# Kernel tuning notes

Measured on AMD Instinct MI355X. Metric: run time of the kernel, lower is better.

The kernel has to match this reference:

```python
import jax, jax.numpy as jnp
import numpy as np

N = 50000      # nodes
E = 800000     # directed edges (avg degree 16)
IN = 96
H = 96
OUT = 96


def _gcn(x, W, b, src, dst, norm, n):
    # PyG GCNConv: h = x @ W; aggregate norm * h[src] at dst; add bias.
    h = x @ W                          # [N, H]
    msg = h[src] * norm[:, None]       # [E+N, H]
    out = jax.ops.segment_sum(msg, dst, num_segments=n)
    return out + b


def setup_inputs() -> dict:
    key = jax.random.key(0)
    ks = jax.random.split(key, 12)
    s = 1.0 / np.sqrt(IN)
    sh = 1.0 / np.sqrt(H)
    return {
        "x": jax.random.normal(ks[0], (N, IN), dtype=jnp.float32),
        "edge_index": jax.random.randint(ks[1], (2, E), 0, N, dtype=jnp.int32),
        "W_local": jax.random.uniform(ks[2], (IN, H), jnp.float32, -s, s),
        "b_local": jnp.zeros((H,), jnp.float32),
        "W_g1": jax.random.uniform(ks[3], (IN, H), jnp.float32, -s, s),
        "b_g1": jnp.zeros((H,), jnp.float32),
        "W_g2": jax.random.uniform(ks[4], (H, H), jnp.float32, -sh, sh),
        "b_g2": jnp.zeros((H,), jnp.float32),
        "W_fuse": jax.random.uniform(ks[5], (2 * H, OUT), jnp.float32, -1.0 / np.sqrt(2 * H), 1.0 / np.sqrt(2 * H)),
        "b_fuse": jnp.zeros((OUT,), jnp.float32),
    }


def reference(x, edge_index, W_local, b_local, W_g1, b_g1, W_g2, b_g2, W_fuse, b_fuse):
    n = x.shape[0]
    loops = jnp.arange(n, dtype=edge_index.dtype)
    src = jnp.concatenate([edge_index[0], loops])   # add self-loops (GCNConv default)
    dst = jnp.concatenate([edge_index[1], loops])
    deg = jax.ops.segment_sum(jnp.ones_like(dst, dtype=x.dtype), dst, num_segments=n)
    dis = jax.lax.rsqrt(jnp.maximum(deg, 1.0))      # deg >= 1 due to self-loops
    norm = dis[src] * dis[dst]                      # sym-normalized edge weights

    local = jax.nn.relu(_gcn(x, W_local, b_local, src, dst, norm, n))
    g = jax.nn.relu(_gcn(x, W_g1, b_g1, src, dst, norm, n))
    g = jax.nn.relu(_gcn(g, W_g2, b_g2, src, dst, norm, n))

    combined = jnp.concatenate([local, g], axis=-1)  # [N, 2H]
    return combined @ W_fuse + b_fuse                # [N, OUT]
```

## Files before the change

### kernel.cpp

```cpp
#include <hip/hip_runtime.h>

#define HDIM 96
#define LSTR 104
#define CAP 96

typedef __attribute__((ext_vector_type(8))) short bf16x8;
typedef __attribute__((ext_vector_type(4))) float f32x4;

#define LGKM0() do { asm volatile("s_waitcnt lgkmcnt(0)" ::: "memory"); \
                     __builtin_amdgcn_sched_barrier(0); } while (0)

__device__ __forceinline__ unsigned short bf16rne(float x) {
  const unsigned u = __float_as_uint(x);
  return (unsigned short)((u + 0x7fff + ((u >> 16) & 1)) >> 16);
}

__device__ __forceinline__ void split2(float x, unsigned short& hi, unsigned short& lo) {
  const unsigned u = __float_as_uint(x);
  hi = (unsigned short)(u >> 16);
  const float xhi = __uint_as_float(u & 0xffff0000u);
  lo = (unsigned short)(__float_as_uint(x - xhi) >> 16);
}

__global__ __launch_bounds__(256) void init_k(
    int* __restrict__ indeg, int n, int zb,
    const float* __restrict__ W0, const float* __restrict__ W1,
    const float* __restrict__ W2, const float* __restrict__ W3,
    unsigned short* __restrict__ dH, unsigned short* __restrict__ dL) {
  if (blockIdx.x < zb) {
    const int i = blockIdx.x * 256 + threadIdx.x;
    if (i < n) indeg[i] = 0;
  } else {
    const int t = (blockIdx.x - zb) * 256 + threadIdx.x;
    if (t < 5 * 9216) {
      const int tile = t / 9216, r = t % 9216;
      const int nn = r / 96, k = r % 96;
      const float* W = (tile == 0) ? W0 : (tile == 1) ? W1 : (tile == 2) ? W2 : W3;
      const int row = (tile == 4) ? 96 + k : k;
      unsigned short h, l;
      split2(W[row * 96 + nn], h, l);
      dH[t] = h;
      dL[t] = l;
    }
  }
}

__global__ __launch_bounds__(256) void place_k(
    const int* __restrict__ src, const int* __restrict__ dst,
    int* __restrict__ indeg, unsigned short* __restrict__ csr_src, int e) {
  const int base = blockIdx.x * 1024 + threadIdx.x;
  int s[4], d[4], slot[4];
  bool ok[4];
#pragma unroll
  for (int j = 0; j < 4; j++) {
    const int i = base + j * 256;
    ok[j] = (i < e);
    s[j] = ok[j] ? src[i] : 0;
    d[j] = ok[j] ? dst[i] : 0;
  }
#pragma unroll
  for (int j = 0; j < 4; j++)
    if (ok[j]) slot[j] = atomicAdd(&indeg[d[j]], 1);
#pragma unroll
  for (int j = 0; j < 4; j++)
    if (ok[j] && slot[j] < CAP)
      csr_src[d[j] * CAP + slot[j]] = (unsigned short)s[j];
}

__global__ __launch_bounds__(256) void scale_k(
    const int* __restrict__ indeg, const float* __restrict__ x,
    unsigned short* __restrict__ msgX, float* __restrict__ dis, int n) {
  const int t = blockIdx.x * 256 + threadIdx.x;
  if (t < n) dis[t] = rsqrtf((float)(1 + indeg[t]));
  if (t >= n * 24) return;
  const float dd = rsqrtf((float)(1 + indeg[t / 24]));
  const float4 v = ((const float4*)x)[t];
  ushort4 h;
  h.x = bf16rne(v.x * dd); h.y = bf16rne(v.y * dd);
  h.z = bf16rne(v.z * dd); h.w = bf16rne(v.w * dd);
  ((ushort4*)msgX)[t] = h;
}

__device__ __forceinline__ void acc8(float* a, uint4 p) {
  a[0] += __uint_as_float(p.x << 16);
  a[1] += __uint_as_float(p.x & 0xffff0000u);
  a[2] += __uint_as_float(p.y << 16);
  a[3] += __uint_as_float(p.y & 0xffff0000u);
  a[4] += __uint_as_float(p.z << 16);
  a[5] += __uint_as_float(p.z & 0xffff0000u);
  a[6] += __uint_as_float(p.w << 16);
  a[7] += __uint_as_float(p.w & 0xffff0000u);
}

__device__ __forceinline__ void gather_x4p(const unsigned short* __restrict__ csr,
                                           int i, int end,
                                           const unsigned short* __restrict__ hp,
                                           int quad, float a[3][8]) {
  const int q8 = 8 * quad;
  int s0 = 0, s1 = 0, s2 = 0, s3 = 0;
  if (i + 3 < end) { s0 = csr[i]; s1 = csr[i + 1]; s2 = csr[i + 2]; s3 = csr[i + 3]; }
  while (i + 3 < end) {
    const unsigned short* p0 = hp + (size_t)s0 * HDIM + q8;
    const unsigned short* p1 = hp + (size_t)s1 * HDIM + q8;
    const unsigned short* p2 = hp + (size_t)s2 * HDIM + q8;
    const unsigned short* p3 = hp + (size_t)s3 * HDIM + q8;
    const uint4 v00 = *(const uint4*)(p0), v01 = *(const uint4*)(p0 + 32), v02 = *(const uint4*)(p0 + 64);
    const uint4 v10 = *(const uint4*)(p1), v11 = *(const uint4*)(p1 + 32), v12 = *(const uint4*)(p1 + 64);
    const uint4 v20 = *(const uint4*)(p2), v21 = *(const uint4*)(p2 + 32), v22 = *(const uint4*)(p2 + 64);
    const uint4 v30 = *(const uint4*)(p3), v31 = *(const uint4*)(p3 + 32), v32 = *(const uint4*)(p3 + 64);
    i += 4;
    if (i + 3 < end) { s0 = csr[i]; s1 = csr[i + 1]; s2 = csr[i + 2]; s3 = csr[i + 3]; }
    acc8(a[0], v00); acc8(a[1], v01); acc8(a[2], v02);
    acc8(a[0], v10); acc8(a[1], v11); acc8(a[2], v12);
    acc8(a[0], v20); acc8(a[1], v21); acc8(a[2], v22);
    acc8(a[0], v30); acc8(a[1], v31); acc8(a[2], v32);
  }
  for (; i < end; i++) {
    const unsigned short* p = hp + (size_t)csr[i] * HDIM + q8;
    acc8(a[0], *(const uint4*)p);
    acc8(a[1], *(const uint4*)(p + 32));
    acc8(a[2], *(const uint4*)(p + 64));
  }
}

__device__ __forceinline__ void flush_tile(const unsigned short* TB,
                                           unsigned short* __restrict__ g,
                                           int row0w, int M, int lane) {
  const int rr = lane >> 2, sb = lane & 3;
  const int grow = row0w + rr;
#pragma unroll
  for (int j = 0; j < 3; j++) {
    const int slot = sb + 4 * j;
    const uint4 v = *(const uint4*)(&TB[rr * LSTR + slot * 8]);
    if (grow < M) *(uint4*)(&g[(size_t)grow * HDIM + slot * 8]) = v;
  }
}

template<bool DUAL, bool FUSE>
__global__ __launch_bounds__(256) void gat_gemm_k(
    const unsigned short* __restrict__ csr_src, const int* __restrict__ indeg,
    const float* __restrict__ dis, const unsigned short* __restrict__ hp,
    const unsigned short* __restrict__ WH0, const unsigned short* __restrict__ WL0,
    const float* __restrict__ b0,
    const unsigned short* __restrict__ WH1, const unsigned short* __restrict__ WL1,
    const float* __restrict__ b1,
    unsigned short* __restrict__ outH, unsigned short* __restrict__ outL,
    unsigned short* __restrict__ outMsg,
    const unsigned short* __restrict__ WH2, const unsigned short* __restrict__ WL2,
    const unsigned short* __restrict__ AH2, const unsigned short* __restrict__ AL2,
    const float* __restrict__ bF, float* __restrict__ fout, int M) {
  __shared__ __align__(16) unsigned short Wh[96 * LSTR], Wl[96 * LSTR];
  __shared__ __align__(16) unsigned short TBUF[4][16 * LSTR];
  const int t = threadIdx.x;
  const int lane = t & 63, wv = t >> 6;
  const int m = lane & 15, quad = lane >> 4;
  const int row0 = blockIdx.x * 64;
  const int node = row0 + 16 * wv + m;
  unsigned short* TB = TBUF[wv];

  for (int u = t; u < 1152; u += 256) {
    const int nn = u / 12, kq = u % 12;
    *(uint4*)(&Wh[nn * LSTR + 8 * kq]) = ((const uint4*)(WH0 + (size_t)nn * HDIM))[kq];
    *(uint4*)(&Wl[nn * LSTR + 8 * kq]) = ((const uint4*)(WL0 + (size_t)nn * HDIM))[kq];
  }

  float a[3][8];
#pragma unroll
  for (int c = 0; c < 3; c++)
#pragma unroll
    for (int jj = 0; jj < 8; jj++) a[c][jj] = 0.f;
  if (node < M) {
    const float dd = dis[node];
    const int cnt = min(indeg[node], CAP);
    const int beg = node * CAP;
    const int end = beg + cnt;
    const unsigned short* selfp = hp + (size_t)node * HDIM + 8 * quad;
    const uint4 sv0 = *(const uint4*)(selfp);
    const uint4 sv1 = *(const uint4*)(selfp + 32);
    const uint4 sv2 = *(const uint4*)(selfp + 64);
    gather_x4p(csr_src, beg, end, hp, quad, a);
    acc8(a[0], sv0); acc8(a[1], sv1); acc8(a[2], sv2);
#pragma unroll
    for (int c = 0; c < 3; c++)
#pragma unroll
      for (int jj = 0; jj < 8; jj++) a[c][jj] *= dd;
  }
  bf16x8 ah[3], al[3];
#pragma unroll
  for (int c = 0; c < 3; c++)
#pragma unroll
    for (int jj = 0; jj < 8; jj++) {
      unsigned short h, l;
      split2(a[c][jj], h, l);
      ah[c][jj] = (short)h;
      al[c][jj] = (short)l;
    }

  bf16x8 lh[3], ll[3];
  if (FUSE) {
#pragma unroll
    for (int kc = 0; kc < 3; kc++) { lh[kc] = (bf16x8){0,0,0,0,0,0,0,0}; ll[kc] = lh[kc]; }
    if (node < M) {
      const unsigned short* ph = AH2 + (size_t)node * HDIM + 8 * quad;
      const unsigned short* pl = AL2 + (size_t)node * HDIM + 8 * quad;
#pragma unroll
      for (int kc = 0; kc < 3; kc++) {
        lh[kc] = *(const bf16x8*)(ph + 32 * kc);
        ll[kc] = *(const bf16x8*)(pl + 32 * kc);
      }
    }
  }

  __syncthreads();

  f32x4 acc0[6];
#pragma unroll
  for (int c = 0; c < 6; c++) acc0[c] = (f32x4){0.f, 0.f, 0.f, 0.f};
#pragma unroll
  for (int kc = 0; kc < 3; kc++) {
    const int ko = 32 * kc + 8 * quad;
#pragma unroll
    for (int c = 0; c < 6; c++) {
      const bf16x8 wh = *(const bf16x8*)(&Wh[(16 * c + m) * LSTR + ko]);
      const bf16x8 wl = *(const bf16x8*)(&Wl[(16 * c + m) * LSTR + ko]);
      acc0[c] = __builtin_amdgcn_mfma_f32_16x16x32_bf16(ah[kc], wh, acc0[c], 0, 0, 0);
      acc0[c] = __builtin_amdgcn_mfma_f32_16x16x32_bf16(ah[kc], wl, acc0[c], 0, 0, 0);
      acc0[c] = __builtin_amdgcn_mfma_f32_16x16x32_bf16(al[kc], wh, acc0[c], 0, 0, 0);
    }
  }

  const int row0w = row0 + 16 * wv;

  if (!FUSE) {
#pragma unroll
    for (int c = 0; c < 6; c++) {
      const float bv = b0[16 * c + m];
#pragma unroll
      for (int r = 0; r < 4; r++) {
        const float v = fmaxf(acc0[c][r] + bv, 0.f);
        unsigned short h, l;
        split2(v, h, l);
        (void)l;
        TB[(4 * quad + r) * LSTR + 16 * c + m] = h;
      }
    }
    LGKM0();
    flush_tile(TB, outH, row0w, M, lane);
    LGKM0();
#pragma unroll
    for (int c = 0; c < 6; c++) {
      const float bv = b0[16 * c + m];
#pragma unroll
      for (int r = 0; r < 4; r++) {
        const float v = fmaxf(acc0[c][r] + bv, 0.f);
        unsigned short h, l;
        split2(v, h, l);
        (void)h;
        TB[(4 * quad + r) * LSTR + 16 * c + m] = l;
      }
    }
    LGKM0();
    flush_tile(TB, outL, row0w, M, lane);
    LGKM0();
  }

  if (DUAL) {
    __syncthreads();
    for (int u = t; u < 1152; u += 256) {
      const int nn = u / 12, kq = u % 12;
      *(uint4*)(&Wh[nn * LSTR + 8 * kq]) = ((const uint4*)(WH1 + (size_t)nn * HDIM))[kq];
      *(uint4*)(&Wl[nn * LSTR + 8 * kq]) = ((const uint4*)(WL1 + (size_t)nn * HDIM))[kq];
    }
    __syncthreads();
    f32x4 acc1[6];
#pragma unroll
    for (int c = 0; c < 6; c++) acc1[c] = (f32x4){0.f, 0.f, 0.f, 0.f};
#pragma unroll
    for (int kc = 0; kc < 3; kc++) {
      const int ko = 32 * kc + 8 * quad;
#pragma unroll
      for (int c = 0; c < 6; c++) {
        const bf16x8 wh = *(const bf16x8*)(&Wh[(16 * c + m) * LSTR + ko]);
        const bf16x8 wl = *(const bf16x8*)(&Wl[(16 * c + m) * LSTR + ko]);
        acc1[c] = __builtin_amdgcn_mfma_f32_16x16x32_bf16(ah[kc], wh, acc1[c], 0, 0, 0);
        acc1[c] = __builtin_amdgcn_mfma_f32_16x16x32_bf16(ah[kc], wl, acc1[c], 0, 0, 0);
        acc1[c] = __builtin_amdgcn_mfma_f32_16x16x32_bf16(al[kc], wh, acc1[c], 0, 0, 0);
      }
    }
    float dv[4];
#pragma unroll
    for (int r = 0; r < 4; r++) dv[r] = (row0w + 4 * quad + r < M) ? dis[row0w + 4 * quad + r] : 0.f;
#pragma unroll
    for (int c = 0; c < 6; c++) {
      const float bv = b1[16 * c + m];
#pragma unroll
      for (int r = 0; r < 4; r++)
        TB[(4 * quad + r) * LSTR + 16 * c + m] =
            bf16rne(fmaxf(acc1[c][r] + bv, 0.f) * dv[r]);
    }
    LGKM0();
    flush_tile(TB, outMsg, row0w, M, lane);
  }

  if (FUSE) {
    bf16x8 gh[3], gl[3];
#pragma unroll
    for (int c = 0; c < 6; c++) {
      const float bv = b0[16 * c + m];
#pragma unroll
      for (int r = 0; r < 4; r++) {
        const float v = fmaxf(acc0[c][r] + bv, 0.f);
        unsigned short h, l;
        split2(v, h, l);
        (void)l;
        TB[(4 * quad + r) * LSTR + 16 * c + m] = h;
      }
    }
    LGKM0();
#pragma unroll
    for (int kc = 0; kc < 3; kc++)
      gh[kc] = *(const bf16x8*)(&TB[m * LSTR + 32 * kc + 8 * quad]);
    LGKM0();
#pragma unroll
    for (int c = 0; c < 6; c++) {
      const float bv = b0[16 * c + m];
#pragma unroll
      for (int r = 0; r < 4; r++) {
        const float v = fmaxf(acc0[c][r] + bv, 0.f);
        unsigned short h, l;
        split2(v, h, l);
        (void)h;
        TB[(4 * quad + r) * LSTR + 16 * c + m] = l;
      }
    }
    LGKM0();
#pragma unroll
    for (int kc = 0; kc < 3; kc++)
      gl[kc] = *(const bf16x8*)(&TB[m * LSTR + 32 * kc + 8 * quad]);
    LGKM0();

    f32x4 accF[6];
#pragma unroll
    for (int c = 0; c < 6; c++) accF[c] = (f32x4){0.f, 0.f, 0.f, 0.f};

    __syncthreads();
    for (int u = t; u < 1152; u += 256) {
      const int nn = u / 12, kq = u % 12;
      *(uint4*)(&Wh[nn * LSTR + 8 * kq]) = ((const uint4*)(WH1 + (size_t)nn * HDIM))[kq];
      *(uint4*)(&Wl[nn * LSTR + 8 * kq]) = ((const uint4*)(WL1 + (size_t)nn * HDIM))[kq];
    }
    __syncthreads();
#pragma unroll
    for (int kc = 0; kc < 3; kc++) {
      const int ko = 32 * kc + 8 * quad;
#pragma unroll
      for (int c = 0; c < 6; c++) {
        const bf16x8 wh = *(const bf16x8*)(&Wh[(16 * c + m) * LSTR + ko]);
        const bf16x8 wl = *(const bf16x8*)(&Wl[(16 * c + m) * LSTR + ko]);
        accF[c] = __builtin_amdgcn_mfma_f32_16x16x32_bf16(lh[kc], wh, accF[c], 0, 0, 0);
        accF[c] = __builtin_amdgcn_mfma_f32_16x16x32_bf16(lh[kc], wl, accF[c], 0, 0, 0);
        accF[c] = __builtin_amdgcn_mfma_f32_16x16x32_bf16(ll[kc], wh, accF[c], 0, 0, 0);
      }
    }
    __syncthreads();
    for (int u = t; u < 1152; u += 256) {
      const int nn = u / 12, kq = u % 12;
      *(uint4*)(&Wh[nn * LSTR + 8 * kq]) = ((const uint4*)(WH2 + (size_t)nn * HDIM))[kq];
      *(uint4*)(&Wl[nn * LSTR + 8 * kq]) = ((const uint4*)(WL2 + (size_t)nn * HDIM))[kq];
    }
    __syncthreads();
#pragma unroll
    for (int kc = 0; kc < 3; kc++) {
      const int ko = 32 * kc + 8 * quad;
#pragma unroll
      for (int c = 0; c < 6; c++) {
        const bf16x8 wh = *(const bf16x8*)(&Wh[(16 * c + m) * LSTR + ko]);
        const bf16x8 wl = *(const bf16x8*)(&Wl[(16 * c + m) * LSTR + ko]);
        accF[c] = __builtin_amdgcn_mfma_f32_16x16x32_bf16(gh[kc], wh, accF[c], 0, 0, 0);
        accF[c] = __builtin_amdgcn_mfma_f32_16x16x32_bf16(gh[kc], wl, accF[c], 0, 0, 0);
        accF[c] = __builtin_amdgcn_mfma_f32_16x16x32_bf16(gl[kc], wh, accF[c], 0, 0, 0);
      }
    }

    float* TBf = (float*)TB;
    const int rr = lane >> 2, sb = lane & 3;
    const int grow = row0w + rr;
#pragma unroll
    for (int half = 0; half < 2; half++) {
#pragma unroll
      for (int c = 0; c < 3; c++) {
        const int cc = 3 * half + c;
        const float bv = bF[16 * cc + m];
#pragma unroll
        for (int r = 0; r < 4; r++)
          TBf[(4 * quad + r) * 52 + 16 * c + m] = accF[cc][r] + bv;
      }
      LGKM0();
#pragma unroll
      for (int j = 0; j < 3; j++) {
        const int slot = sb + 4 * j;
        const float4 v = *(const float4*)(&TBf[rr * 52 + slot * 4]);
        if (grow < M) *(float4*)(&fout[(size_t)grow * HDIM + half * 48 + slot * 4]) = v;
      }
      LGKM0();
    }
  }
}

extern "C" void kernel_launch(void* const* d_in, const int* in_sizes, int n_in,
                              void* d_out, int out_size, void* d_ws, size_t ws_size,
                              hipStream_t stream) {
  const float* x       = (const float*)d_in[0];
  const int*   edge    = (const int*)d_in[1];
  const float* W_local = (const float*)d_in[2];
  const float* b_local = (const float*)d_in[3];
  const float* W_g1    = (const float*)d_in[4];
  const float* b_g1    = (const float*)d_in[5];
  const float* W_g2    = (const float*)d_in[6];
  const float* b_g2    = (const float*)d_in[7];
  const float* W_fuse  = (const float*)d_in[8];
  const float* b_fuse  = (const float*)d_in[9];
  float* out = (float*)d_out;

  const int n = in_sizes[0] / HDIM;
  const int e = in_sizes[1] / 2;
  const int* src = edge;
  const int* dst = edge + e;

  char* ws = (char*)d_ws;
  auto alloc = [&](size_t bytes) { char* p = ws; ws += (bytes + 255) & ~(size_t)255; return p; };
  int*   indeg   = (int*)alloc((size_t)n * 4);
  float* dis     = (float*)alloc((size_t)n * 4);
  unsigned short* csr_src = (unsigned short*)alloc((size_t)n * CAP * 2);
  const size_t mat16 = (size_t)n * HDIM * 2;
  unsigned short* msgX = (unsigned short*)alloc(mat16);
  unsigned short* msgG = (unsigned short*)alloc(mat16);
  unsigned short* locH = (unsigned short*)alloc(mat16);
  unsigned short* locL = (unsigned short*)alloc(mat16);
  unsigned short* wH   = (unsigned short*)alloc(5 * 9216 * 2);
  unsigned short* wL   = (unsigned short*)alloc(5 * 9216 * 2);

  const int zb = (n + 255) / 256;
  init_k<<<zb + 180, 256, 0, stream>>>(indeg, n, zb,
                                       W_local, W_g1, W_g2, W_fuse, wH, wL);
  place_k<<<(e + 1023) / 1024, 256, 0, stream>>>(src, dst, indeg, csr_src, e);
  scale_k<<<(n * 24 + 255) / 256, 256, 0, stream>>>(indeg, x, msgX, dis, n);

  const int gb = (n + 63) / 64;

  gat_gemm_k<true, false><<<gb, 256, 0, stream>>>(csr_src, indeg, dis, msgX,
                                                  wH, wL, b_local,
                                                  wH + 9216, wL + 9216, b_g1,
                                                  locH, locL, msgG,
                                                  nullptr, nullptr, nullptr, nullptr,
                                                  nullptr, nullptr, n);
  gat_gemm_k<false, true><<<gb, 256, 0, stream>>>(csr_src, indeg, dis, msgG,
                                                  wH + 2 * 9216, wL + 2 * 9216, b_g2,
                                                  wH + 3 * 9216, wL + 3 * 9216, nullptr,
                                                  nullptr, nullptr, nullptr,
                                                  wH + 4 * 9216, wL + 4 * 9216,
                                                  locH, locL, b_fuse, out, n);
}
```

Baseline: 228.3 us.

## Sort nodes by in-degree via histogram permutation to balance gather work per wave

Builds a degree histogram and a counting-sort permutation of nodes by in-degree, then has the gather+GEMM kernels process nodes in permuted order and scatter results back through the permutation. Lanes in a wave then hold nodes of similar degree, which cuts divergence from uneven gather loop lengths. In exchange it adds a scatter kernel, extra global atomics and indirect reads and writes, and it loses the locality of contiguous node rows in the output stores.

```diff
diff --git a/kernel.cpp b/kernel.cpp
--- a/kernel.cpp
+++ b/kernel.cpp
@@ -22,16 +22,31 @@
   lo = (unsigned short)(__float_as_uint(x - xhi) >> 16);
 }
 
+__device__ __forceinline__ int wave_incl_scan(int v, int lane) {
+#pragma unroll
+  for (int off = 1; off < 64; off <<= 1) {
+    int t = __shfl_up(v, off, 64);
+    if (lane >= off) v += t;
+  }
+  return v;
+}
+
 __global__ __launch_bounds__(256) void init_k(
     int* __restrict__ indeg, int n, int zb,
+    int* __restrict__ hist, int* __restrict__ hcur,
     const float* __restrict__ W0, const float* __restrict__ W1,
     const float* __restrict__ W2, const float* __restrict__ W3,
     unsigned short* __restrict__ dH, unsigned short* __restrict__ dL) {
+  const int tid = threadIdx.x;
+  if (blockIdx.x == 0) {
+    if (tid < 64) hist[tid] = 0;
+    else if (tid < 128) hcur[tid - 64] = 0;
+  }
   if (blockIdx.x < zb) {
-    const int i = blockIdx.x * 256 + threadIdx.x;
+    const int i = blockIdx.x * 256 + tid;
     if (i < n) indeg[i] = 0;
   } else {
-    const int t = (blockIdx.x - zb) * 256 + threadIdx.x;
+    const int t = (blockIdx.x - zb) * 256 + tid;
     if (t < 5 * 9216) {
       const int tile = t / 9216, r = t % 9216;
       const int nn = r / 96, k = r % 96;
@@ -69,16 +84,51 @@
 
 __global__ __launch_bounds__(256) void scale_k(
     const int* __restrict__ indeg, const float* __restrict__ x,
-    unsigned short* __restrict__ msgX, float* __restrict__ dis, int n) {
-  const int t = blockIdx.x * 256 + threadIdx.x;
+    unsigned short* __restrict__ msgX, float* __restrict__ dis,
+    int* __restrict__ hist, int n) {
+  __shared__ int lh[64];
+  const int tid = threadIdx.x;
+  const int t = blockIdx.x * 256 + tid;
+  const bool hblk = (blockIdx.x * 256 < n);
+  if (hblk) {
+    if (tid < 64) lh[tid] = 0;
+    __syncthreads();
+    if (t < n) atomicAdd(&lh[min(indeg[t], 63)], 1);
+    __syncthreads();
+    if (tid < 64 && lh[tid] > 0) atomicAdd(&hist[tid], lh[tid]);
+  }
   if (t < n) dis[t] = rsqrtf((float)(1 + indeg[t]));
-  if (t >= n * 24) return;
-  const float dd = rsqrtf((float)(1 + indeg[t / 24]));
-  const float4 v = ((const float4*)x)[t];
-  ushort4 h;
-  h.x = bf16rne(v.x * dd); h.y = bf16rne(v.y * dd);
-  h.z = bf16rne(v.z * dd); h.w = bf16rne(v.w * dd);
-  ((ushort4*)msgX)[t] = h;
+  if (t < n * 24) {
+    const float dd = rsqrtf((float)(1 + indeg[t / 24]));
+    const float4 v = ((const float4*)x)[t];
+    ushort4 h;
+    h.x = bf16rne(v.x * dd); h.y = bf16rne(v.y * dd);
+    h.z = bf16rne(v.z * dd); h.w = bf16rne(v.w * dd);
+    ((ushort4*)msgX)[t] = h;
+  }
+}
+
+__global__ __launch_bounds__(256) void scatter_k(
+    const int* __restrict__ indeg, const int* __restrict__ hist,
+    int* __restrict__ hcur, int* __restrict__ perm, int n) {
+  __shared__ int hb[64], lh[64], lbase[64];
+  const int tid = threadIdx.x;
+  if (tid < 64) {
+    const int v = hist[tid];
+    hb[tid] = wave_incl_scan(v, tid) - v;
+    lh[tid] = 0;
+  }
+  __syncthreads();
+  const int i = blockIdx.x * 256 + tid;
+  int bin = 0, loc = 0;
+  if (i < n) {
+    bin = min(indeg[i], 63);
+    loc = atomicAdd(&lh[bin], 1);
+  }
+  __syncthreads();
+  if (tid < 64 && lh[tid] > 0) lbase[tid] = atomicAdd(&hcur[tid], lh[tid]);
+  __syncthreads();
+  if (i < n) perm[hb[bin] + lbase[bin] + loc] = i;
 }
 
 __device__ __forceinline__ void acc8(float* a, uint4 p) {
@@ -125,14 +175,16 @@
 
 __device__ __forceinline__ void flush_tile(const unsigned short* TB,
                                            unsigned short* __restrict__ g,
+                                           const int* __restrict__ perm,
                                            int row0w, int M, int lane) {
   const int rr = lane >> 2, sb = lane & 3;
-  const int grow = row0w + rr;
+  const int prow = row0w + rr;
+  const int grow = (prow < M) ? perm[prow] : -1;
 #pragma unroll
   for (int j = 0; j < 3; j++) {
     const int slot = sb + 4 * j;
     const uint4 v = *(const uint4*)(&TB[rr * LSTR + slot * 8]);
-    if (grow < M) *(uint4*)(&g[(size_t)grow * HDIM + slot * 8]) = v;
+    if (grow >= 0) *(uint4*)(&g[(size_t)grow * HDIM + slot * 8]) = v;
   }
 }
 
@@ -140,6 +192,7 @@
 __global__ __launch_bounds__(256) void gat_gemm_k(
     const unsigned short* __restrict__ csr_src, const int* __restrict__ indeg,
     const float* __restrict__ dis, const unsigned short* __restrict__ hp,
+    const int* __restrict__ perm,
     const unsigned short* __restrict__ WH0, const unsigned short* __restrict__ WL0,
     const float* __restrict__ b0,
     const unsigned short* __restrict__ WH1, const unsigned short* __restrict__ WL1,
@@ -155,7 +208,9 @@
   const int lane = t & 63, wv = t >> 6;
   const int m = lane & 15, quad = lane >> 4;
   const int row0 = blockIdx.x * 64;
-  const int node = row0 + 16 * wv + m;
+  const int prow = row0 + 16 * wv + m;
+  const bool act = (prow < M);
+  const int node = act ? perm[prow] : 0;
   unsigned short* TB = TBUF[wv];
 
   for (int u = t; u < 1152; u += 256) {
@@ -169,7 +224,7 @@
   for (int c = 0; c < 3; c++)
 #pragma unroll
     for (int jj = 0; jj < 8; jj++) a[c][jj] = 0.f;
-  if (node < M) {
+  if (act) {
     const float dd = dis[node];
     const int cnt = min(indeg[node], CAP);
     const int beg = node * CAP;
@@ -200,7 +255,7 @@
   if (FUSE) {
 #pragma unroll
     for (int kc = 0; kc < 3; kc++) { lh[kc] = (bf16x8){0,0,0,0,0,0,0,0}; ll[kc] = lh[kc]; }
-    if (node < M) {
+    if (act) {
       const unsigned short* ph = AH2 + (size_t)node * HDIM + 8 * quad;
       const unsigned short* pl = AL2 + (size_t)node * HDIM + 8 * quad;
 #pragma unroll
@@ -245,7 +300,7 @@
       }
     }
     LGKM0();
-    flush_tile(TB, outH, row0w, M, lane);
+    flush_tile(TB, outH, perm, row0w, M, lane);
     LGKM0();
 #pragma unroll
     for (int c = 0; c < 6; c++) {
@@ -260,7 +315,7 @@
       }
     }
     LGKM0();
-    flush_tile(TB, outL, row0w, M, lane);
+    flush_tile(TB, outL, perm, row0w, M, lane);
     LGKM0();
   }
 
@@ -289,7 +344,10 @@
     }
     float dv[4];
 #pragma unroll
-    for (int r = 0; r < 4; r++) dv[r] = (row0w + 4 * quad + r < M) ? dis[row0w + 4 * quad + r] : 0.f;
+    for (int r = 0; r < 4; r++) {
+      const int pr = row0w + 4 * quad + r;
+      dv[r] = (pr < M) ? dis[perm[pr]] : 0.f;
+    }
 #pragma unroll
     for (int c = 0; c < 6; c++) {
       const float bv = b1[16 * c + m];
@@ -299,7 +357,7 @@
             bf16rne(fmaxf(acc1[c][r] + bv, 0.f) * dv[r]);
     }
     LGKM0();
-    flush_tile(TB, outMsg, row0w, M, lane);
+    flush_tile(TB, outMsg, perm, row0w, M, lane);
   }
 
   if (FUSE) {
@@ -384,7 +442,8 @@
 
     float* TBf = (float*)TB;
     const int rr = lane >> 2, sb = lane & 3;
-    const int grow = row0w + rr;
+    const int pr2 = row0w + rr;
+    const int grow = (pr2 < M) ? perm[pr2] : -1;
 #pragma unroll
     for (int half = 0; half < 2; half++) {
 #pragma unroll
@@ -400,7 +459,7 @@
       for (int j = 0; j < 3; j++) {
         const int slot = sb + 4 * j;
         const float4 v = *(const float4*)(&TBf[rr * 52 + slot * 4]);
-        if (grow < M) *(float4*)(&fout[(size_t)grow * HDIM + half * 48 + slot * 4]) = v;
+        if (grow >= 0) *(float4*)(&fout[(size_t)grow * HDIM + half * 48 + slot * 4]) = v;
       }
       LGKM0();
     }
@@ -431,6 +490,9 @@
   auto alloc = [&](size_t bytes) { char* p = ws; ws += (bytes + 255) & ~(size_t)255; return p; };
   int*   indeg   = (int*)alloc((size_t)n * 4);
   float* dis     = (float*)alloc((size_t)n * 4);
+  int*   perm    = (int*)alloc((size_t)n * 4);
+  int*   hist    = (int*)alloc(64 * 4);
+  int*   hcur    = (int*)alloc(64 * 4);
   unsigned short* csr_src = (unsigned short*)alloc((size_t)n * CAP * 2);
   const size_t mat16 = (size_t)n * HDIM * 2;
   unsigned short* msgX = (unsigned short*)alloc(mat16);
@@ -441,20 +503,21 @@
   unsigned short* wL   = (unsigned short*)alloc(5 * 9216 * 2);
 
   const int zb = (n + 255) / 256;
-  init_k<<<zb + 180, 256, 0, stream>>>(indeg, n, zb,
+  init_k<<<zb + 180, 256, 0, stream>>>(indeg, n, zb, hist, hcur,
                                        W_local, W_g1, W_g2, W_fuse, wH, wL);
   place_k<<<(e + 1023) / 1024, 256, 0, stream>>>(src, dst, indeg, csr_src, e);
-  scale_k<<<(n * 24 + 255) / 256, 256, 0, stream>>>(indeg, x, msgX, dis, n);
+  scale_k<<<(n * 24 + 255) / 256, 256, 0, stream>>>(indeg, x, msgX, dis, hist, n);
+  scatter_k<<<(n + 255) / 256, 256, 0, stream>>>(indeg, hist, hcur, perm, n);
 
   const int gb = (n + 63) / 64;
 
-  gat_gemm_k<true, false><<<gb, 256, 0, stream>>>(csr_src, indeg, dis, msgX,
+  gat_gemm_k<true, false><<<gb, 256, 0, stream>>>(csr_src, indeg, dis, msgX, perm,
                                                   wH, wL, b_local,
                                                   wH + 9216, wL + 9216, b_g1,
                                                   locH, locL, msgG,
                                                   nullptr, nullptr, nullptr, nullptr,
                                                   nullptr, nullptr, n);
-  gat_gemm_k<false, true><<<gb, 256, 0, stream>>>(csr_src, indeg, dis, msgG,
+  gat_gemm_k<false, true><<<gb, 256, 0, stream>>>(csr_src, indeg, dis, msgG, perm,
                                                   wH + 2 * 9216, wL + 2 * 9216, b_g2,
                                                   wH + 3 * 9216, wL + 3 * 9216, nullptr,
                                                   nullptr, nullptr, nullptr,
```

Result: slower. 236.5 us (+3.6%).
